# Kernel tuning notes

Measured on AMD Instinct MI355X. Metric: run time of the kernel, lower is better.

Reference implementation:

```python
import jax, jax.numpy as jnp
import numpy as np

B, T, D, H, O, L = 64, 512, 256, 512, 1, 4


def _lstm_layer(x, W_ih, W_hh, b_ih, b_hh):
    """Single LSTM layer, batch_first. x: [B,T,in] -> [B,T,H].
    PyTorch gate order: i, f, g, o."""
    Bv = x.shape[0]
    Hv = W_hh.shape[1]
    # Precompute input contribution for all timesteps (one big GEMM).
    gx = jnp.einsum('btd,gd->btg', x, W_ih) + b_ih + b_hh  # [B,T,4H]

    def step(carry, g_t):
        h, c = carry
        z = g_t + h @ W_hh.T  # [B,4H]
        i, f, g, o = jnp.split(z, 4, axis=-1)
        i = jax.nn.sigmoid(i)
        f = jax.nn.sigmoid(f)
        g = jnp.tanh(g)
        o = jax.nn.sigmoid(o)
        c = f * c + i * g
        h = o * jnp.tanh(c)
        return (h, c), h

    h0 = jnp.zeros((Bv, Hv), x.dtype)
    c0 = jnp.zeros((Bv, Hv), x.dtype)
    _, hs = jax.lax.scan(step, (h0, c0), jnp.swapaxes(gx, 0, 1))  # [T,B,H]
    return jnp.swapaxes(hs, 0, 1)  # [B,T,H]


def setup_inputs() -> dict:
    key = jax.random.key(0)
    ks = jax.random.split(key, 19)
    s = 1.0 / np.sqrt(H)  # PyTorch LSTM init scale
    d = {"x": jax.random.normal(ks[0], (B, T, D), jnp.float32)}
    dims = [D, H, H, H]
    i = 1
    for l in range(L):
        d[f"W_ih{l}"] = jax.random.normal(ks[i], (4 * H, dims[l]), jnp.float32) * s; i += 1
        d[f"W_hh{l}"] = jax.random.normal(ks[i], (4 * H, H), jnp.float32) * s; i += 1
        d[f"b_ih{l}"] = jax.random.normal(ks[i], (4 * H,), jnp.float32) * s; i += 1
        d[f"b_hh{l}"] = jax.random.normal(ks[i], (4 * H,), jnp.float32) * s; i += 1
    d["W_out"] = jax.random.normal(ks[17], (O, H), jnp.float32) * s
    d["b_out"] = jax.random.normal(ks[18], (O,), jnp.float32) * s
    return d


def reference(x, W_ih0, W_hh0, b_ih0, b_hh0,
              W_ih1, W_hh1, b_ih1, b_hh1,
              W_ih2, W_hh2, b_ih2, b_hh2,
              W_ih3, W_hh3, b_ih3, b_hh3,
              W_out, b_out):
    h = x
    layers = ((W_ih0, W_hh0, b_ih0, b_hh0),
              (W_ih1, W_hh1, b_ih1, b_hh1),
              (W_ih2, W_hh2, b_ih2, b_hh2),
              (W_ih3, W_hh3, b_ih3, b_hh3))
    for Wih, Whh, bih, bhh in layers:
        h = _lstm_layer(h, Wih, Whh, bih, bhh)
    # Linear head on last timestep
    return h[:, -1, :] @ W_out.T + b_out  # [B, O]
```

## Files before the change

### kernel.cpp

```cpp
#include <hip/hip_runtime.h>
#include <hip/hip_fp16.h>

typedef _Float16 h16;
typedef _Float16 v8h  __attribute__((ext_vector_type(8)));
typedef float    v4f  __attribute__((ext_vector_type(4)));

#define NPROD 16u

struct PParams {
  const float* x;
  const float* Wih[4];
  const float* Whh[4];
  const float* bih[4];
  const float* bhh[4];
  h16* s[4];
  unsigned int* flags;
};

__device__ inline float fsigmoid(float x){
  float e = __builtin_amdgcn_exp2f(-1.4426950408889634f * __builtin_fabsf(x));
  float r = __builtin_amdgcn_rcpf(1.0f + e);
  return x >= 0.f ? r : e * r;
}
__device__ inline float ftanhf(float x){
  float e = __builtin_amdgcn_exp2f(-2.8853900817779268f * __builtin_fabsf(x));
  float t = (1.0f - e) * __builtin_amdgcn_rcpf(1.0f + e);
  return x >= 0.f ? t : -t;
}

__device__ inline unsigned int fload(const unsigned int* p){
  return __hip_atomic_load(p, __ATOMIC_RELAXED, __HIP_MEMORY_SCOPE_AGENT);
}
__device__ inline unsigned long long cload64(const void* p){
  return __hip_atomic_load((const unsigned long long*)p, __ATOMIC_RELAXED,
                           __HIP_MEMORY_SCOPE_AGENT);
}
__device__ inline void cstore32(void* p, unsigned int v){
  __hip_atomic_store((unsigned int*)p, v, __ATOMIC_RELAXED, __HIP_MEMORY_SCOPE_AGENT);
}

__device__ inline void wait_flag(const unsigned int* f, unsigned int tgt){
  int it = 0;
  while (fload(f) < tgt){
    __builtin_amdgcn_s_sleep(1);
    if (++it > (1 << 21)) break;
  }
}

template<int KIN, bool XSRC>
__device__ void run_layer(const float* __restrict__ Wih, const float* __restrict__ Whh,
                          const float* __restrict__ bih, const float* __restrict__ bhh,
                          const float* __restrict__ xsrc,
                          const h16* __restrict__ src,
                          h16* __restrict__ dst, int dstMask,
                          unsigned int* flagSelf, unsigned int* flagSrc,
                          int rg, int bg, h16* A)
{
  const int tid  = threadIdx.x;
  const int wv   = tid >> 6;
  const int lane = tid & 63;
  const int ISTR = KIN + 8;
  const int HOFF = 8320;
  const int KI   = KIN / 32;

  const int n16  = lane & 15;
  const int unit = rg*32 + wv*8 + (n16 & 7);
  const int ksub = ((lane >> 4) & 3) * 8;
  const int row0 = ((n16 >> 3)    ) * 512 + unit;
  const int row1 = ((n16 >> 3) + 2) * 512 + unit;

  v8h wihf[KI][2];
  v8h whhf[16][2];
  #pragma unroll
  for (int kk = 0; kk < KI; ++kk){
    #pragma unroll
    for (int j = 0; j < 2; ++j){
      const float* p = Wih + (size_t)(j ? row1 : row0) * KIN + kk*32 + ksub;
      v8h fr;
      #pragma unroll
      for (int e = 0; e < 8; ++e) fr[e] = (h16)p[e];
      wihf[kk][j] = fr;
    }
  }
  #pragma unroll
  for (int kk = 0; kk < 16; ++kk){
    #pragma unroll
    for (int j = 0; j < 2; ++j){
      const float* p = Whh + (size_t)(j ? row1 : row0) * 512 + kk*32 + ksub;
      v8h fr;
      #pragma unroll
      for (int e = 0; e < 8; ++e) fr[e] = (h16)p[e];
      whhf[kk][j] = fr;
    }
  }
  const float bias0 = bih[row0] + bhh[row0];
  const float bias1 = bih[row1] + bhh[row1];
  float c[4] = {0.f, 0.f, 0.f, 0.f};
  const bool hi = (lane & 8) != 0;

  #pragma unroll 1
  for (int t = 0; t < 512; ++t){
    if (!XSRC && tid == 0) wait_flag(flagSrc + t, NPROD);
    __syncthreads();

    if (XSRC){
      #pragma unroll
      for (int i = 0; i < 2; ++i){
        int q = tid + i*256;
        int row = q >> 5, col = q & 31;
        const float* xp = xsrc + ((size_t)(bg*16 + row)*512 + t)*256 + col*8;
        float4 v0 = *(const float4*)(xp);
        float4 v1 = *(const float4*)(xp + 4);
        v8h o = {(h16)v0.x,(h16)v0.y,(h16)v0.z,(h16)v0.w,
                 (h16)v1.x,(h16)v1.y,(h16)v1.z,(h16)v1.w};
        *(v8h*)(A + row*ISTR + col*8) = o;
      }
    } else {
      unsigned long long a0[4], a1[4];
      #pragma unroll
      for (int i = 0; i < 4; ++i){
        int q = tid + i*256;
        int row = q >> 6, col = q & 63;
        const h16* sp = src + ((size_t)t*64 + bg*16 + row)*512 + col*8;
        a0[i] = cload64(sp);
        a1[i] = cload64(sp + 4);
      }
      #pragma unroll
      for (int i = 0; i < 4; ++i){
        int q = tid + i*256;
        int row = q >> 6, col = q & 63;
        union { unsigned long long u[2]; v8h h; } tmp;
        tmp.u[0] = a0[i]; tmp.u[1] = a1[i];
        *(v8h*)(A + row*ISTR + col*8) = tmp.h;
      }
    }
    __syncthreads();

    unsigned int pre = NPROD;
    if (tid == 0 && t > 0) pre = fload(flagSelf + t - 1);

    v4f acc0 = {0.f, 0.f, 0.f, 0.f};
    v4f acc1 = {0.f, 0.f, 0.f, 0.f};
    const h16* Ain = A + n16*ISTR + ksub;
    #pragma unroll
    for (int kk = 0; kk < KI; ++kk){
      v8h a = *(const v8h*)(Ain + kk*32);
      acc0 = __builtin_amdgcn_mfma_f32_16x16x32_f16(a, wihf[kk][0], acc0, 0, 0, 0);
      acc1 = __builtin_amdgcn_mfma_f32_16x16x32_f16(a, wihf[kk][1], acc1, 0, 0, 0);
    }

    if (tid == 0 && t > 0 && pre < NPROD) wait_flag(flagSelf + t - 1, NPROD);
    __syncthreads();

    if (t == 0){
      #pragma unroll
      for (int i = 0; i < 4; ++i){
        int q = tid + i*256;
        int row = q >> 6, col = q & 63;
        union { unsigned long long u[2]; v8h h; } tmp;
        tmp.u[0] = 0ull; tmp.u[1] = 0ull;
        *(v8h*)(A + HOFF + row*520 + col*8) = tmp.h;
      }
    } else {
      const h16* hsrc = dst + (size_t)((t-1) & dstMask) * 64 * 512;
      unsigned long long a0[4], a1[4];
      #pragma unroll
      for (int i = 0; i < 4; ++i){
        int q = tid + i*256;
        int row = q >> 6, col = q & 63;
        const h16* sp = hsrc + (size_t)(bg*16 + row)*512 + col*8;
        a0[i] = cload64(sp);
        a1[i] = cload64(sp + 4);
      }
      #pragma unroll
      for (int i = 0; i < 4; ++i){
        int q = tid + i*256;
        int row = q >> 6, col = q & 63;
        union { unsigned long long u[2]; v8h h; } tmp;
        tmp.u[0] = a0[i]; tmp.u[1] = a1[i];
        *(v8h*)(A + HOFF + row*520 + col*8) = tmp.h;
      }
    }
    __syncthreads();

    const h16* Ah = A + HOFF + n16*520 + ksub;
    #pragma unroll
    for (int kk = 0; kk < 16; ++kk){
      v8h a = *(const v8h*)(Ah + kk*32);
      acc0 = __builtin_amdgcn_mfma_f32_16x16x32_f16(a, whhf[kk][0], acc0, 0, 0, 0);
      acc1 = __builtin_amdgcn_mfma_f32_16x16x32_f16(a, whhf[kk][1], acc1, 0, 0, 0);
    }

    h16* drow = dst + (size_t)(t & dstMask) * 64 * 512;
    #pragma unroll
    for (int r = 0; r < 4; ++r){
      float z0 = acc0[r] + bias0;
      float z1 = acc1[r] + bias1;
      float p0 = __shfl_xor(z0, 8, 64);
      float p1 = __shfl_xor(z1, 8, 64);
      float iv = hi ? p0 : z0;
      float fv = hi ? z0 : p0;
      float gv = hi ? p1 : z1;
      float ov = hi ? z1 : p1;
      iv = fsigmoid(iv); fv = fsigmoid(fv); ov = fsigmoid(ov);
      gv = ftanhf(gv);
      c[r] = fv * c[r] + iv * gv;
      float hval = ov * ftanhf(c[r]);
      h16 hh = (h16)hval;
      unsigned int mine = (unsigned int)__builtin_bit_cast(unsigned short, hh);
      unsigned int partner = (unsigned int)__shfl_xor((int)mine, 1, 64);
      if (!hi && !(n16 & 1)){
        int batch = bg*16 + ((lane >> 4) << 2) + r;
        cstore32((void*)(drow + (size_t)batch*512 + unit), mine | (partner << 16));
      }
    }
    __syncthreads();

    if (tid == 0)
      __hip_atomic_fetch_add(flagSelf + t, 1u, __ATOMIC_RELAXED, __HIP_MEMORY_SCOPE_AGENT);
  }
}

__global__ __launch_bounds__(256, 1) void lstm_persist(PParams p){
  __shared__ h16 A[16640];
  const int bx = blockIdx.x;
  const int l  = bx >> 6;
  const int rg = (bx >> 2) & 15;
  const int bg = bx & 3;
  unsigned int* fl = p.flags + (size_t)(l*4 + bg) * 512;
  if (l == 0){
    run_layer<256, true >(p.Wih[0], p.Whh[0], p.bih[0], p.bhh[0], p.x, nullptr,
                          p.s[0], 511, fl, nullptr, rg, bg, A);
  } else {
    unsigned int* fs = p.flags + (size_t)((l-1)*4 + bg) * 512;
    run_layer<512, false>(p.Wih[l], p.Whh[l], p.bih[l], p.bhh[l], nullptr, p.s[l-1],
                          p.s[l], (l == 3) ? 1 : 511, fl, fs, rg, bg, A);
  }
}

__global__ void head_k(const h16* __restrict__ h3, const float* __restrict__ Wo,
                       const float* __restrict__ bo, float* __restrict__ out){
  const int b = blockIdx.x;
  const int lane = threadIdx.x;
  float s = 0.f;
  for (int u = lane; u < 512; u += 64)
    s += (float)h3[(size_t)b * 512 + u] * Wo[u];
  #pragma unroll
  for (int off = 32; off; off >>= 1) s += __shfl_down(s, off, 64);
  if (lane == 0) out[b] = s + bo[0];
}

__global__ void zero_out_k(float* out, int n){
  int i = blockIdx.x * 64 + threadIdx.x;
  if (i < n) out[i] = 0.f;
}

extern "C" void kernel_launch(void* const* d_in, const int* in_sizes, int n_in,
                              void* d_out, int out_size, void* d_ws, size_t ws_size,
                              hipStream_t stream){
  PParams p;
  p.x = (const float*)d_in[0];
  for (int l = 0; l < 4; ++l){
    p.Wih[l] = (const float*)d_in[1 + 4*l + 0];
    p.Whh[l] = (const float*)d_in[1 + 4*l + 1];
    p.bih[l] = (const float*)d_in[1 + 4*l + 2];
    p.bhh[l] = (const float*)d_in[1 + 4*l + 3];
  }
  const float* Wo = (const float*)d_in[17];
  const float* bo = (const float*)d_in[18];

  const size_t FLAG_BYTES = 4 * 4 * 512 * sizeof(unsigned int);
  const size_t SBYTES     = (size_t)512 * 64 * 512 * 2;
  const size_t NEED       = 32768 + 3 * SBYTES + (size_t)2 * 64 * 512 * 2;

  if (ws_size < NEED){
    zero_out_k<<<dim3(1), dim3(64), 0, stream>>>((float*)d_out, out_size);
    return;
  }

  char* ws = (char*)d_ws;
  p.flags = (unsigned int*)ws;
  size_t off = 32768;
  for (int l = 0; l < 3; ++l){ p.s[l] = (h16*)(ws + off); off += SBYTES; }
  p.s[3] = (h16*)(ws + off);

  hipMemsetAsync(p.flags, 0, FLAG_BYTES, stream);

  void* args[] = { &p };
  hipError_t e = hipLaunchCooperativeKernel((void*)lstm_persist, dim3(256), dim3(256),
                                            args, 0, stream);
  if (e != hipSuccess){
    lstm_persist<<<dim3(256), dim3(256), 0, stream>>>(p);
  }

  head_k<<<dim3(64), dim3(64), 0, stream>>>(p.s[3] + (size_t)64 * 512, Wo, bo, (float*)d_out);
}
```

Before: 1.977 ms.

## Replace block barriers and LDS staging with per-wave flags and direct fragment loads

Each wave now loads its MFMA A-fragments for the input and hidden projections straight from global memory instead of staging them in shared memory behind several block-wide barriers. Step completion moves from one atomic counter per timestep to one per-wave slot per layer and batch group, polled wave-wide with __all. The input projection for step t+1 is computed right after step t's h is stored, so it overlaps the wait for other waves. Accumulators are split into even and odd chains to give the MFMA pipeline more independent work. The cost is redundant global reads per wave and a weaker ordering guarantee, since only a vmcnt wait precedes the relaxed flag store.

```diff
diff --git a/kernel.cpp b/kernel.cpp
--- a/kernel.cpp
+++ b/kernel.cpp
@@ -4,8 +4,6 @@
 typedef _Float16 h16;
 typedef _Float16 v8h  __attribute__((ext_vector_type(8)));
 typedef float    v4f  __attribute__((ext_vector_type(4)));
-
-#define NPROD 16u
 
 struct PParams {
   const float* x;
@@ -39,9 +37,11 @@
   __hip_atomic_store((unsigned int*)p, v, __ATOMIC_RELAXED, __HIP_MEMORY_SCOPE_AGENT);
 }
 
-__device__ inline void wait_flag(const unsigned int* f, unsigned int tgt){
+__device__ inline void wait_group(const unsigned int* slots, unsigned int tgt, int lane){
   int it = 0;
-  while (fload(f) < tgt){
+  while (true){
+    unsigned int v = fload(slots + lane);
+    if (__all(v >= tgt)) break;
     __builtin_amdgcn_s_sleep(1);
     if (++it > (1 << 21)) break;
   }
@@ -53,14 +53,12 @@
                           const float* __restrict__ xsrc,
                           const h16* __restrict__ src,
                           h16* __restrict__ dst, int dstMask,
-                          unsigned int* flagSelf, unsigned int* flagSrc,
-                          int rg, int bg, h16* A)
+                          unsigned int* flagSelf, const unsigned int* flagSrc,
+                          int rg, int bg)
 {
   const int tid  = threadIdx.x;
   const int wv   = tid >> 6;
   const int lane = tid & 63;
-  const int ISTR = KIN + 8;
-  const int HOFF = 8320;
   const int KI   = KIN / 32;
 
   const int n16  = lane & 15;
@@ -70,7 +68,6 @@
   const int row1 = ((n16 >> 3) + 2) * 512 + unit;
 
   v8h wihf[KI][2];
-  v8h whhf[16][2];
   #pragma unroll
   for (int kk = 0; kk < KI; ++kk){
     #pragma unroll
@@ -82,6 +79,7 @@
       wihf[kk][j] = fr;
     }
   }
+  v8h whhf[16][2];
   #pragma unroll
   for (int kk = 0; kk < 16; ++kk){
     #pragma unroll
@@ -96,106 +94,76 @@
   const float bias0 = bih[row0] + bhh[row0];
   const float bias1 = bih[row1] + bhh[row1];
   float c[4] = {0.f, 0.f, 0.f, 0.f};
-  const bool hi = (lane & 8) != 0;
+  const bool hi   = (lane & 8) != 0;
+  const int slot  = rg*4 + wv;
+  const int abatch = bg*16 + n16;
+
+  v4f a0e = {0,0,0,0}, a0o = {0,0,0,0}, a1e = {0,0,0,0}, a1o = {0,0,0,0};
+
+  auto wih_tile = [&](int t, v4f& e0, v4f& o0, v4f& e1, v4f& o1){
+    if constexpr (XSRC){
+      const float* xp = xsrc + ((size_t)abatch*512 + t)*256 + ksub;
+      #pragma unroll
+      for (int kk = 0; kk < KI; ++kk){
+        float4 v0 = *(const float4*)(xp + kk*32);
+        float4 v1 = *(const float4*)(xp + kk*32 + 4);
+        v8h a = {(h16)v0.x,(h16)v0.y,(h16)v0.z,(h16)v0.w,
+                 (h16)v1.x,(h16)v1.y,(h16)v1.z,(h16)v1.w};
+        if (kk & 1){
+          o0 = __builtin_amdgcn_mfma_f32_16x16x32_f16(a, wihf[kk][0], o0, 0, 0, 0);
+          o1 = __builtin_amdgcn_mfma_f32_16x16x32_f16(a, wihf[kk][1], o1, 0, 0, 0);
+        } else {
+          e0 = __builtin_amdgcn_mfma_f32_16x16x32_f16(a, wihf[kk][0], e0, 0, 0, 0);
+          e1 = __builtin_amdgcn_mfma_f32_16x16x32_f16(a, wihf[kk][1], e1, 0, 0, 0);
+        }
+      }
+    } else {
+      const h16* sp = src + ((size_t)t*64 + abatch)*512 + ksub;
+      #pragma unroll
+      for (int kk = 0; kk < KI; ++kk){
+        union { unsigned long long u[2]; v8h h; } tmp;
+        tmp.u[0] = cload64(sp + kk*32);
+        tmp.u[1] = cload64(sp + kk*32 + 4);
+        if (kk & 1){
+          o0 = __builtin_amdgcn_mfma_f32_16x16x32_f16(tmp.h, wihf[kk][0], o0, 0, 0, 0);
+          o1 = __builtin_amdgcn_mfma_f32_16x16x32_f16(tmp.h, wihf[kk][1], o1, 0, 0, 0);
+        } else {
+          e0 = __builtin_amdgcn_mfma_f32_16x16x32_f16(tmp.h, wihf[kk][0], e0, 0, 0, 0);
+          e1 = __builtin_amdgcn_mfma_f32_16x16x32_f16(tmp.h, wihf[kk][1], e1, 0, 0, 0);
+        }
+      }
+    }
+  };
+
+  if constexpr (!XSRC) wait_group(flagSrc, 1u, lane);
+  wih_tile(0, a0e, a0o, a1e, a1o);
 
   #pragma unroll 1
   for (int t = 0; t < 512; ++t){
-    if (!XSRC && tid == 0) wait_flag(flagSrc + t, NPROD);
-    __syncthreads();
-
-    if (XSRC){
-      #pragma unroll
-      for (int i = 0; i < 2; ++i){
-        int q = tid + i*256;
-        int row = q >> 5, col = q & 31;
-        const float* xp = xsrc + ((size_t)(bg*16 + row)*512 + t)*256 + col*8;
-        float4 v0 = *(const float4*)(xp);
-        float4 v1 = *(const float4*)(xp + 4);
-        v8h o = {(h16)v0.x,(h16)v0.y,(h16)v0.z,(h16)v0.w,
-                 (h16)v1.x,(h16)v1.y,(h16)v1.z,(h16)v1.w};
-        *(v8h*)(A + row*ISTR + col*8) = o;
-      }
-    } else {
-      unsigned long long a0[4], a1[4];
-      #pragma unroll
-      for (int i = 0; i < 4; ++i){
-        int q = tid + i*256;
-        int row = q >> 6, col = q & 63;
-        const h16* sp = src + ((size_t)t*64 + bg*16 + row)*512 + col*8;
-        a0[i] = cload64(sp);
-        a1[i] = cload64(sp + 4);
-      }
-      #pragma unroll
-      for (int i = 0; i < 4; ++i){
-        int q = tid + i*256;
-        int row = q >> 6, col = q & 63;
+    if (t > 0){
+      wait_group(flagSelf, (unsigned)t, lane);
+      const h16* hp = dst + (size_t)((t-1) & dstMask) * 64 * 512
+                          + (size_t)abatch * 512 + ksub;
+      #pragma unroll
+      for (int kk = 0; kk < 16; ++kk){
         union { unsigned long long u[2]; v8h h; } tmp;
-        tmp.u[0] = a0[i]; tmp.u[1] = a1[i];
-        *(v8h*)(A + row*ISTR + col*8) = tmp.h;
-      }
-    }
-    __syncthreads();
-
-    unsigned int pre = NPROD;
-    if (tid == 0 && t > 0) pre = fload(flagSelf + t - 1);
-
-    v4f acc0 = {0.f, 0.f, 0.f, 0.f};
-    v4f acc1 = {0.f, 0.f, 0.f, 0.f};
-    const h16* Ain = A + n16*ISTR + ksub;
-    #pragma unroll
-    for (int kk = 0; kk < KI; ++kk){
-      v8h a = *(const v8h*)(Ain + kk*32);
-      acc0 = __builtin_amdgcn_mfma_f32_16x16x32_f16(a, wihf[kk][0], acc0, 0, 0, 0);
-      acc1 = __builtin_amdgcn_mfma_f32_16x16x32_f16(a, wihf[kk][1], acc1, 0, 0, 0);
-    }
-
-    if (tid == 0 && t > 0 && pre < NPROD) wait_flag(flagSelf + t - 1, NPROD);
-    __syncthreads();
-
-    if (t == 0){
-      #pragma unroll
-      for (int i = 0; i < 4; ++i){
-        int q = tid + i*256;
-        int row = q >> 6, col = q & 63;
-        union { unsigned long long u[2]; v8h h; } tmp;
-        tmp.u[0] = 0ull; tmp.u[1] = 0ull;
-        *(v8h*)(A + HOFF + row*520 + col*8) = tmp.h;
-      }
-    } else {
-      const h16* hsrc = dst + (size_t)((t-1) & dstMask) * 64 * 512;
-      unsigned long long a0[4], a1[4];
-      #pragma unroll
-      for (int i = 0; i < 4; ++i){
-        int q = tid + i*256;
-        int row = q >> 6, col = q & 63;
-        const h16* sp = hsrc + (size_t)(bg*16 + row)*512 + col*8;
-        a0[i] = cload64(sp);
-        a1[i] = cload64(sp + 4);
-      }
-      #pragma unroll
-      for (int i = 0; i < 4; ++i){
-        int q = tid + i*256;
-        int row = q >> 6, col = q & 63;
-        union { unsigned long long u[2]; v8h h; } tmp;
-        tmp.u[0] = a0[i]; tmp.u[1] = a1[i];
-        *(v8h*)(A + HOFF + row*520 + col*8) = tmp.h;
-      }
-    }
-    __syncthreads();
-
-    const h16* Ah = A + HOFF + n16*520 + ksub;
-    #pragma unroll
-    for (int kk = 0; kk < 16; ++kk){
-      v8h a = *(const v8h*)(Ah + kk*32);
-      acc0 = __builtin_amdgcn_mfma_f32_16x16x32_f16(a, whhf[kk][0], acc0, 0, 0, 0);
-      acc1 = __builtin_amdgcn_mfma_f32_16x16x32_f16(a, whhf[kk][1], acc1, 0, 0, 0);
+        tmp.u[0] = cload64(hp + kk*32);
+        tmp.u[1] = cload64(hp + kk*32 + 4);
+        if (kk & 1){
+          a0o = __builtin_amdgcn_mfma_f32_16x16x32_f16(tmp.h, whhf[kk][0], a0o, 0, 0, 0);
+          a1o = __builtin_amdgcn_mfma_f32_16x16x32_f16(tmp.h, whhf[kk][1], a1o, 0, 0, 0);
+        } else {
+          a0e = __builtin_amdgcn_mfma_f32_16x16x32_f16(tmp.h, whhf[kk][0], a0e, 0, 0, 0);
+          a1e = __builtin_amdgcn_mfma_f32_16x16x32_f16(tmp.h, whhf[kk][1], a1e, 0, 0, 0);
+        }
+      }
     }
 
     h16* drow = dst + (size_t)(t & dstMask) * 64 * 512;
     #pragma unroll
     for (int r = 0; r < 4; ++r){
-      float z0 = acc0[r] + bias0;
-      float z1 = acc1[r] + bias1;
+      float z0 = a0e[r] + a0o[r] + bias0;
+      float z1 = a1e[r] + a1o[r] + bias1;
       float p0 = __shfl_xor(z0, 8, 64);
       float p1 = __shfl_xor(z1, 8, 64);
       float iv = hi ? p0 : z0;
@@ -214,27 +182,32 @@
         cstore32((void*)(drow + (size_t)batch*512 + unit), mine | (partner << 16));
       }
     }
-    __syncthreads();
-
-    if (tid == 0)
-      __hip_atomic_fetch_add(flagSelf + t, 1u, __ATOMIC_RELAXED, __HIP_MEMORY_SCOPE_AGENT);
+
+    asm volatile("s_waitcnt vmcnt(0)" ::: "memory");
+    if (lane == 0) cstore32(flagSelf + slot, (unsigned)(t + 1));
+
+    if (t < 511){
+      a0e = (v4f){0,0,0,0}; a0o = (v4f){0,0,0,0};
+      a1e = (v4f){0,0,0,0}; a1o = (v4f){0,0,0,0};
+      if constexpr (!XSRC) wait_group(flagSrc, (unsigned)(t + 2), lane);
+      wih_tile(t + 1, a0e, a0o, a1e, a1o);
+    }
   }
 }
 
 __global__ __launch_bounds__(256, 1) void lstm_persist(PParams p){
-  __shared__ h16 A[16640];
   const int bx = blockIdx.x;
   const int l  = bx >> 6;
   const int rg = (bx >> 2) & 15;
   const int bg = bx & 3;
-  unsigned int* fl = p.flags + (size_t)(l*4 + bg) * 512;
+  unsigned int* fl = p.flags + (size_t)(l*4 + bg) * 64;
   if (l == 0){
     run_layer<256, true >(p.Wih[0], p.Whh[0], p.bih[0], p.bhh[0], p.x, nullptr,
-                          p.s[0], 511, fl, nullptr, rg, bg, A);
+                          p.s[0], 511, fl, nullptr, rg, bg);
   } else {
-    unsigned int* fs = p.flags + (size_t)((l-1)*4 + bg) * 512;
+    const unsigned int* fs = p.flags + (size_t)((l-1)*4 + bg) * 64;
     run_layer<512, false>(p.Wih[l], p.Whh[l], p.bih[l], p.bhh[l], nullptr, p.s[l-1],
-                          p.s[l], (l == 3) ? 1 : 511, fl, fs, rg, bg, A);
+                          p.s[l], (l == 3) ? 1 : 511, fl, fs, rg, bg);
   }
 }
 
@@ -269,7 +242,7 @@
   const float* Wo = (const float*)d_in[17];
   const float* bo = (const float*)d_in[18];
 
-  const size_t FLAG_BYTES = 4 * 4 * 512 * sizeof(unsigned int);
+  const size_t FLAG_BYTES = 16 * 64 * sizeof(unsigned int);
   const size_t SBYTES     = (size_t)512 * 64 * 512 * 2;
   const size_t NEED       = 32768 + 3 * SBYTES + (size_t)2 * 64 * 512 * 2;
 
```

Result: slower. 5.256 ms (+165.9%).

## Replace per-block atomic counters with per-wave progress slots and split MFMA accumulators

Applied to the files above, without the earlier changes.

Each wave now publishes its own progress by storing the timestep count into a dedicated slot, and all lanes of a wave poll the 64 producer slots together with __all. This replaces the thread-0 spin loops, the atomic fetch-add, and several block-wide __syncthreads. The MFMA accumulation is also split into even and odd chains so consecutive matrix ops do not depend on each other. The cost is more polling traffic per wave and a weaker ordering argument, since a wave can pass the wait before its sibling waves in the same block are ready.

```diff
diff --git a/kernel.cpp b/kernel.cpp
--- a/kernel.cpp
+++ b/kernel.cpp
@@ -4,8 +4,6 @@
 typedef _Float16 h16;
 typedef _Float16 v8h  __attribute__((ext_vector_type(8)));
 typedef float    v4f  __attribute__((ext_vector_type(4)));
-
-#define NPROD 16u
 
 struct PParams {
   const float* x;
@@ -39,12 +37,15 @@
   __hip_atomic_store((unsigned int*)p, v, __ATOMIC_RELAXED, __HIP_MEMORY_SCOPE_AGENT);
 }
 
-__device__ inline void wait_flag(const unsigned int* f, unsigned int tgt){
+__device__ inline void wait_slots(const unsigned int* slots, unsigned int tgt, int lane){
+  unsigned int v = fload(slots + lane);
+  if (__all(v >= tgt)) return;
   int it = 0;
-  while (fload(f) < tgt){
+  do {
     __builtin_amdgcn_s_sleep(1);
-    if (++it > (1 << 21)) break;
-  }
+    v = fload(slots + lane);
+    if (++it > (1 << 20)) break;
+  } while (!__all(v >= tgt));
 }
 
 template<int KIN, bool XSRC>
@@ -53,7 +54,7 @@
                           const float* __restrict__ xsrc,
                           const h16* __restrict__ src,
                           h16* __restrict__ dst, int dstMask,
-                          unsigned int* flagSelf, unsigned int* flagSrc,
+                          unsigned int* flagSelf, const unsigned int* flagSrc,
                           int rg, int bg, h16* A)
 {
   const int tid  = threadIdx.x;
@@ -70,7 +71,6 @@
   const int row1 = ((n16 >> 3) + 2) * 512 + unit;
 
   v8h wihf[KI][2];
-  v8h whhf[16][2];
   #pragma unroll
   for (int kk = 0; kk < KI; ++kk){
     #pragma unroll
@@ -82,6 +82,7 @@
       wihf[kk][j] = fr;
     }
   }
+  v8h whhf[16][2];
   #pragma unroll
   for (int kk = 0; kk < 16; ++kk){
     #pragma unroll
@@ -96,14 +97,14 @@
   const float bias0 = bih[row0] + bhh[row0];
   const float bias1 = bih[row1] + bhh[row1];
   float c[4] = {0.f, 0.f, 0.f, 0.f};
-  const bool hi = (lane & 8) != 0;
+  const bool hi   = (lane & 8) != 0;
+  const int  slot = rg*4 + wv;
 
   #pragma unroll 1
   for (int t = 0; t < 512; ++t){
-    if (!XSRC && tid == 0) wait_flag(flagSrc + t, NPROD);
-    __syncthreads();
-
-    if (XSRC){
+    if constexpr (!XSRC) wait_slots(flagSrc, (unsigned)(t + 1), lane);
+
+    if constexpr (XSRC){
       #pragma unroll
       for (int i = 0; i < 2; ++i){
         int q = tid + i*256;
@@ -136,21 +137,26 @@
     }
     __syncthreads();
 
-    unsigned int pre = NPROD;
-    if (tid == 0 && t > 0) pre = fload(flagSelf + t - 1);
-
-    v4f acc0 = {0.f, 0.f, 0.f, 0.f};
-    v4f acc1 = {0.f, 0.f, 0.f, 0.f};
+    unsigned int selfv = 0xffffffffu;
+    if (t > 0) selfv = fload(flagSelf + lane);
+
+    v4f a0e = {0,0,0,0}, a0o = {0,0,0,0};
+    v4f a1e = {0,0,0,0}, a1o = {0,0,0,0};
     const h16* Ain = A + n16*ISTR + ksub;
     #pragma unroll
     for (int kk = 0; kk < KI; ++kk){
       v8h a = *(const v8h*)(Ain + kk*32);
-      acc0 = __builtin_amdgcn_mfma_f32_16x16x32_f16(a, wihf[kk][0], acc0, 0, 0, 0);
-      acc1 = __builtin_amdgcn_mfma_f32_16x16x32_f16(a, wihf[kk][1], acc1, 0, 0, 0);
-    }
-
-    if (tid == 0 && t > 0 && pre < NPROD) wait_flag(flagSelf + t - 1, NPROD);
-    __syncthreads();
+      if (kk & 1){
+        a0o = __builtin_amdgcn_mfma_f32_16x16x32_f16(a, wihf[kk][0], a0o, 0, 0, 0);
+        a1o = __builtin_amdgcn_mfma_f32_16x16x32_f16(a, wihf[kk][1], a1o, 0, 0, 0);
+      } else {
+        a0e = __builtin_amdgcn_mfma_f32_16x16x32_f16(a, wihf[kk][0], a0e, 0, 0, 0);
+        a1e = __builtin_amdgcn_mfma_f32_16x16x32_f16(a, wihf[kk][1], a1e, 0, 0, 0);
+      }
+    }
+
+    if (t > 0 && !__all(selfv >= (unsigned)t))
+      wait_slots(flagSelf, (unsigned)t, lane);
 
     if (t == 0){
       #pragma unroll
@@ -187,15 +193,20 @@
     #pragma unroll
     for (int kk = 0; kk < 16; ++kk){
       v8h a = *(const v8h*)(Ah + kk*32);
-      acc0 = __builtin_amdgcn_mfma_f32_16x16x32_f16(a, whhf[kk][0], acc0, 0, 0, 0);
-      acc1 = __builtin_amdgcn_mfma_f32_16x16x32_f16(a, whhf[kk][1], acc1, 0, 0, 0);
+      if (kk & 1){
+        a0o = __builtin_amdgcn_mfma_f32_16x16x32_f16(a, whhf[kk][0], a0o, 0, 0, 0);
+        a1o = __builtin_amdgcn_mfma_f32_16x16x32_f16(a, whhf[kk][1], a1o, 0, 0, 0);
+      } else {
+        a0e = __builtin_amdgcn_mfma_f32_16x16x32_f16(a, whhf[kk][0], a0e, 0, 0, 0);
+        a1e = __builtin_amdgcn_mfma_f32_16x16x32_f16(a, whhf[kk][1], a1e, 0, 0, 0);
+      }
     }
 
     h16* drow = dst + (size_t)(t & dstMask) * 64 * 512;
     #pragma unroll
     for (int r = 0; r < 4; ++r){
-      float z0 = acc0[r] + bias0;
-      float z1 = acc1[r] + bias1;
+      float z0 = a0e[r] + a0o[r] + bias0;
+      float z1 = a1e[r] + a1o[r] + bias1;
       float p0 = __shfl_xor(z0, 8, 64);
       float p1 = __shfl_xor(z1, 8, 64);
       float iv = hi ? p0 : z0;
@@ -214,10 +225,9 @@
         cstore32((void*)(drow + (size_t)batch*512 + unit), mine | (partner << 16));
       }
     }
-    __syncthreads();
-
-    if (tid == 0)
-      __hip_atomic_fetch_add(flagSelf + t, 1u, __ATOMIC_RELAXED, __HIP_MEMORY_SCOPE_AGENT);
+
+    asm volatile("s_waitcnt vmcnt(0)" ::: "memory");
+    if (lane == 0) cstore32(flagSelf + slot, (unsigned)(t + 1));
   }
 }
 
@@ -227,12 +237,12 @@
   const int l  = bx >> 6;
   const int rg = (bx >> 2) & 15;
   const int bg = bx & 3;
-  unsigned int* fl = p.flags + (size_t)(l*4 + bg) * 512;
+  unsigned int* fl = p.flags + (size_t)(l*4 + bg) * 64;
   if (l == 0){
     run_layer<256, true >(p.Wih[0], p.Whh[0], p.bih[0], p.bhh[0], p.x, nullptr,
                           p.s[0], 511, fl, nullptr, rg, bg, A);
   } else {
-    unsigned int* fs = p.flags + (size_t)((l-1)*4 + bg) * 512;
+    const unsigned int* fs = p.flags + (size_t)((l-1)*4 + bg) * 64;
     run_layer<512, false>(p.Wih[l], p.Whh[l], p.bih[l], p.bhh[l], nullptr, p.s[l-1],
                           p.s[l], (l == 3) ? 1 : 511, fl, fs, rg, bg, A);
   }
@@ -269,7 +279,7 @@
   const float* Wo = (const float*)d_in[17];
   const float* bo = (const float*)d_in[18];
 
-  const size_t FLAG_BYTES = 4 * 4 * 512 * sizeof(unsigned int);
+  const size_t FLAG_BYTES = 16 * 64 * sizeof(unsigned int);
   const size_t SBYTES     = (size_t)512 * 64 * 512 * 2;
   const size_t NEED       = 32768 + 3 * SBYTES + (size_t)2 * 64 * 512 * 2;
 
```

Result: slower. 2.546 ms (+28.8%).
